# Optimization experiments

Hardware: AMD Instinct MI355X
Metric: run time of the kernel (lower is better)

Reference implementation:

```python
import jax, jax.numpy as jnp
import numpy as np
import math

INPUT_DIM = 1024
QUERY_DIM = 1024
VALUE_DIM = 1024

def setup_inputs() -> dict:
    key = jax.random.key(0)
    ks = jax.random.split(key, 7)
    N, T, D = 4, 4096, INPUT_DIM
    s_in = 1.0 / math.sqrt(D)
    X = jax.random.normal(ks[0], (N, T, D), dtype=jnp.float32)
    # torch.nn.Linear weights: (out, in), init ~ U(-1/sqrt(in), 1/sqrt(in))
    Wq = jax.random.uniform(ks[1], (QUERY_DIM, D), jnp.float32, -s_in, s_in)
    bq = jax.random.uniform(ks[2], (QUERY_DIM,), jnp.float32, -s_in, s_in)
    Wk = jax.random.uniform(ks[3], (QUERY_DIM, D), jnp.float32, -s_in, s_in)
    bk = jax.random.uniform(ks[4], (QUERY_DIM,), jnp.float32, -s_in, s_in)
    Wv = jax.random.uniform(ks[5], (VALUE_DIM, D), jnp.float32, -s_in, s_in)
    bv = jax.random.uniform(ks[6], (VALUE_DIM,), jnp.float32, -s_in, s_in)
    return {"X": X, "Wq": Wq, "bq": bq, "Wk": Wk, "bk": bk, "Wv": Wv, "bv": bv}

def reference(X, Wq, bq, Wk, bk, Wv, bv):
    N, T, D = X.shape
    q = jnp.einsum('ntd,qd->ntq', X, Wq) + bq  # (N,T,Q)
    k = jnp.einsum('ntd,qd->ntq', X, Wk) + bk  # (N,T,Q)
    v = jnp.einsum('ntd,vd->ntv', X, Wv) + bv  # (N,T,V)
    # NOTE: original scales by sqrt(D) = sqrt(input_dim), not sqrt(query_dim)
    scores = jnp.einsum('ntq,nsq->nts', q, k) / jnp.sqrt(jnp.asarray(D, X.dtype))
    attn = jax.nn.softmax(scores, axis=-1)  # (N,T,T)
    return jnp.einsum('nts,nsv->ntv', attn, v)
```

## Files before the change

kernel.cpp:

```cpp
#include <hip/hip_runtime.h>
#include <stdint.h>

typedef unsigned short u16;
typedef unsigned char u8;
typedef unsigned int u32;
typedef short shortx8 __attribute__((ext_vector_type(8)));
typedef float floatx4 __attribute__((ext_vector_type(4)));
typedef int intx4 __attribute__((ext_vector_type(4)));
typedef int intx8 __attribute__((ext_vector_type(8)));

__device__ __forceinline__ u16 f2bf(float f) {
    u32 u = __builtin_bit_cast(u32, f);
    u = (u + 0x7fffu + ((u >> 16) & 1u)) >> 16;
    return (u16)u;
}

#if defined(__has_builtin)
#  if __has_builtin(__builtin_amdgcn_cvt_pk_fp8_f32)
#    define HAVE_CVT_FP8 1
#  endif
#  if __has_builtin(__builtin_amdgcn_global_load_lds)
#    define HAVE_GLL 1
#  endif
#endif
#ifndef HAVE_CVT_FP8
#  define HAVE_CVT_FP8 0
#endif
#ifndef HAVE_GLL
#  define HAVE_GLL 0
#endif

__device__ __forceinline__ u8 f2fp8(float f) {
#if HAVE_CVT_FP8
    return (u8)(__builtin_amdgcn_cvt_pk_fp8_f32(f, f, 0, false) & 0xff);
#else
    u32 u = __builtin_bit_cast(u32, f);
    u32 s = (u >> 24) & 0x80u;
    u32 m = u & 0x7fffffffu;
    if (m >= 0x43e00000u) return (u8)(s | 0x7eu);
    if (m < 0x3c800000u) {
        int q = __float2int_rn(__builtin_bit_cast(float, m) * 512.f);
        return (u8)(s | (u32)q);
    }
    u32 r = m + 0x7ffffu + ((m >> 20) & 1u);
    u32 code = (((r >> 23) - 120u) << 3) | ((r >> 20) & 7u);
    if (code > 0x7eu) code = 0x7eu;
    return (u8)(s | code);
#endif
}

#if HAVE_GLL
__device__ __forceinline__ void gload_lds16(const void* g, void* l) {
    __builtin_amdgcn_global_load_lds(
        (const __attribute__((address_space(1))) u32*)g,
        (__attribute__((address_space(3))) u32*)l,
        16, 0, 0);
}
#endif

template <typename OutT, int MODE, int SWZ>
__global__ __launch_bounds__(256, 2) void gemm_bt(
    const u16* __restrict__ Ag, const u16* __restrict__ Bg, OutT* __restrict__ Cg,
    int lda, int ldb, int ldc, int K,
    const float* __restrict__ aux, float scale,
    long long sAz, long long sBz, long long sCz, long long sXz,
    int swz_nhalf)
{
    __shared__ u16 smem[4][128 * 32];

    int z, mb, nb;
    if constexpr (SWZ) {
        const int f = blockIdx.x, xcd = f & 7, g = f >> 3;
        z = xcd >> 1;
        mb = g & 31;
        nb = (xcd & 1) * swz_nhalf + (g >> 5);
    } else {
        z = blockIdx.z; mb = blockIdx.y; nb = blockIdx.x;
    }
    const int m0 = mb * 128, n0 = nb * 128;

    const u16* A = Ag + (long long)z * sAz;
    const u16* B = Bg + (long long)z * sBz;
    OutT* C = Cg + (long long)z * sCz;
    const float* auxp = aux ? aux + (long long)z * sXz : nullptr;

    const int tid = threadIdx.x, lane = tid & 63, wv = tid >> 6;

    const int srow = lane >> 2;
    const int schunk = (lane & 3) * 8;
    const u16* gA0 = A + (size_t)(m0 + wv * 16 + srow) * lda + schunk;
    const u16* gA1 = gA0 + (size_t)64 * lda;
    const u16* gB0 = B + (size_t)(n0 + wv * 16 + srow) * ldb + schunk;
    const u16* gB1 = gB0 + (size_t)64 * ldb;
    const int wb = wv * 512;

    const int wm = (wv & 1) * 64, wn = (wv >> 1) * 64;
    const int mi = lane & 15, kq = lane >> 4;

    floatx4 acc[4][4] = {};

    for (int k0 = 0; k0 < K; k0 += 64) {
#if HAVE_GLL
        gload_lds16(gA0,      &smem[0][wb]);
        gload_lds16(gA1,      &smem[0][2048 + wb]);
        gload_lds16(gA0 + 32, &smem[1][wb]);
        gload_lds16(gA1 + 32, &smem[1][2048 + wb]);
        gload_lds16(gB0,      &smem[2][wb]);
        gload_lds16(gB1,      &smem[2][2048 + wb]);
        gload_lds16(gB0 + 32, &smem[3][wb]);
        gload_lds16(gB1 + 32, &smem[3][2048 + wb]);
#else
        *(shortx8*)(&smem[0][wb] + lane * 8)        = *(const shortx8*)gA0;
        *(shortx8*)(&smem[0][2048 + wb] + lane * 8) = *(const shortx8*)gA1;
        *(shortx8*)(&smem[1][wb] + lane * 8)        = *(const shortx8*)(gA0 + 32);
        *(shortx8*)(&smem[1][2048 + wb] + lane * 8) = *(const shortx8*)(gA1 + 32);
        *(shortx8*)(&smem[2][wb] + lane * 8)        = *(const shortx8*)gB0;
        *(shortx8*)(&smem[2][2048 + wb] + lane * 8) = *(const shortx8*)gB1;
        *(shortx8*)(&smem[3][wb] + lane * 8)        = *(const shortx8*)(gB0 + 32);
        *(shortx8*)(&smem[3][2048 + wb] + lane * 8) = *(const shortx8*)(gB1 + 32);
#endif
        gA0 += 64; gA1 += 64; gB0 += 64; gB1 += 64;
        __syncthreads();

#pragma unroll
        for (int h = 0; h < 2; h++) {
            const u16* Ap = smem[h];
            const u16* Bp = smem[2 + h];
            shortx8 af[4], bfr[4];
#pragma unroll
            for (int i = 0; i < 4; i++)
                af[i] = *(const shortx8*)(Ap + (wm + i * 16 + mi) * 32 + kq * 8);
#pragma unroll
            for (int j = 0; j < 4; j++)
                bfr[j] = *(const shortx8*)(Bp + (wn + j * 16 + mi) * 32 + kq * 8);
#pragma unroll
            for (int i = 0; i < 4; i++)
#pragma unroll
                for (int j = 0; j < 4; j++)
                    acc[i][j] = __builtin_amdgcn_mfma_f32_16x16x32_bf16(
                        af[i], bfr[j], acc[i][j], 0, 0, 0);
        }
        __syncthreads();
    }

    float cb[4];
    if constexpr (MODE == 1) {
#pragma unroll
        for (int j = 0; j < 4; j++) cb[j] = auxp[n0 + wn + j * 16 + mi];
    }

    if constexpr (sizeof(OutT) == 2) {
        u16* ct = &smem[0][0];
#pragma unroll
        for (int i = 0; i < 4; i++) {
#pragma unroll
            for (int r = 0; r < 4; r++) {
                const int lrow = wm + i * 16 + kq * 4 + r;
                float radd = 0.f;
                if constexpr (MODE == 2) radd = auxp[m0 + lrow];
#pragma unroll
                for (int j = 0; j < 4; j++) {
                    float v = acc[i][j][r];
                    if constexpr (MODE == 1) v += cb[j];
                    if constexpr (MODE == 2) v += radd;
                    ct[lrow * 128 + wn + j * 16 + mi] = f2bf(v);
                }
            }
        }
        __syncthreads();
#pragma unroll
        for (int it = 0; it < 8; it++) {
            const int fl = (it * 256 + tid) * 8;
            const int row = fl >> 7, col = fl & 127;
            *(uint4*)(C + (size_t)(m0 + row) * ldc + n0 + col) =
                *(const uint4*)(ct + fl);
        }
    } else if constexpr (sizeof(OutT) == 1) {
        u8* ct = (u8*)&smem[0][0];
#pragma unroll
        for (int i = 0; i < 4; i++) {
#pragma unroll
            for (int r = 0; r < 4; r++) {
                const int lrow = wm + i * 16 + kq * 4 + r;
#pragma unroll
                for (int j = 0; j < 4; j++) {
                    float v = acc[i][j][r];
                    if constexpr (MODE == 1) v += cb[j];
                    ct[lrow * 128 + wn + j * 16 + mi] = f2fp8(v);
                }
            }
        }
        __syncthreads();
        u8* base = (u8*)Cg + ((size_t)mb * 16 + nb) * 16384;
#pragma unroll
        for (int it = 0; it < 4; it++) {
            const int fl = (it * 256 + tid) * 16;
            const int row = fl >> 7, c = (fl >> 4) & 7;
            *(uint4*)(base + row * 128 + ((c ^ (row & 7)) << 4)) =
                *(const uint4*)(ct + fl);
        }
    } else {
#pragma unroll
        for (int i = 0; i < 4; i++) {
#pragma unroll
            for (int r = 0; r < 4; r++) {
                const int row = m0 + wm + i * 16 + kq * 4 + r;
                float rmul = 1.f;
                if constexpr (MODE == 4) rmul = 1.0f / auxp[row];
                OutT* crow = C + (size_t)row * ldc;
#pragma unroll
                for (int j = 0; j < 4; j++) {
                    const int col = n0 + wn + j * 16 + mi;
                    crow[col] = acc[i][j][r] * rmul;
                }
            }
        }
    }
}

__device__ __forceinline__ intx8 cat8(intx4 a, intx4 b) {
    return __builtin_shufflevector(a, b, 0, 1, 2, 3, 4, 5, 6, 7);
}

template <int SWZ>
__global__ __launch_bounds__(256, 1) void gemm_fp8_scores(
    const u8* __restrict__ QKt, u16* __restrict__ Pg,
    float* __restrict__ sums, float scale, int T)
{
    __shared__ u8 smem[2][16384];

    int z, mb, nb;
    if constexpr (SWZ) {
        const int f = blockIdx.x, xcd = f & 7, g = f >> 3;
        z = xcd >> 1;
        mb = g & 31;
        nb = (xcd & 1) * 16 + (g >> 5);
    } else {
        z = blockIdx.z; mb = blockIdx.y; nb = blockIdx.x;
    }
    const int m0 = mb * 128, n0 = nb * 128;

    const u8* At = QKt + ((size_t)(z * 32 + mb) * 16) * 16384;
    const u8* Bt = QKt + ((size_t)(z * 32 + nb) * 16 + 8) * 16384;
    u16* P = Pg + (size_t)z * T * T;
    float* sumz = sums + (size_t)z * T;

    const int tid = threadIdx.x, lane = tid & 63, wv = tid >> 6;
    const int wm = (wv & 1) * 64, wn = (wv >> 1) * 64;
    const int mi = lane & 15, kq = lane >> 4;
    const int xm = mi & 7;
    const int off0 = ((2 * kq) ^ xm) * 16;
    const int off1 = ((2 * kq + 1) ^ xm) * 16;

    const u8* gA = At + wv * 4096 + lane * 16;
    const u8* gB = Bt + wv * 4096 + lane * 16;
    u8* lA = &smem[0][wv * 4096];
    u8* lB = &smem[1][wv * 4096];

    floatx4 acc[4][4] = {};

    for (int kp = 0; kp < 8; kp++) {
#if HAVE_GLL
#pragma unroll
        for (int i = 0; i < 4; i++) {
            gload_lds16(gA + i * 1024, lA + i * 1024);
            gload_lds16(gB + i * 1024, lB + i * 1024);
        }
#else
#pragma unroll
        for (int i = 0; i < 4; i++) {
            *(uint4*)(lA + i * 1024 + lane * 16) = *(const uint4*)(gA + i * 1024);
            *(uint4*)(lB + i * 1024 + lane * 16) = *(const uint4*)(gB + i * 1024);
        }
#endif
        gA += 16384; gB += 16384;
        __syncthreads();

        intx8 af[4];
#pragma unroll
        for (int i = 0; i < 4; i++) {
            const u8* p = &smem[0][(wm + i * 16 + mi) * 128];
            af[i] = cat8(*(const intx4*)(p + off0), *(const intx4*)(p + off1));
        }
#pragma unroll
        for (int j = 0; j < 4; j++) {
            const u8* p = &smem[1][(wn + j * 16 + mi) * 128];
            const intx8 bfr = cat8(*(const intx4*)(p + off0), *(const intx4*)(p + off1));
#pragma unroll
            for (int i = 0; i < 4; i++)
                acc[i][j] = __builtin_amdgcn_mfma_scale_f32_16x16x128_f8f6f4(
                    af[i], bfr, acc[i][j], 0, 0,
                    0, 0x7f7f7f7f, 0, 0x7f7f7f7f);
        }
        __syncthreads();
    }

    u16* ct = (u16*)&smem[0][0];
#pragma unroll
    for (int i = 0; i < 4; i++) {
#pragma unroll
        for (int r = 0; r < 4; r++) {
            const int lrow = wm + i * 16 + kq * 4 + r;
            float rs = 0.f;
#pragma unroll
            for (int j = 0; j < 4; j++) {
                float v = __expf(acc[i][j][r] * scale);
                rs += v;
                ct[lrow * 128 + wn + j * 16 + mi] = f2bf(v);
            }
            rs += __shfl_xor(rs, 1);
            rs += __shfl_xor(rs, 2);
            rs += __shfl_xor(rs, 4);
            rs += __shfl_xor(rs, 8);
            if (mi == 0) atomicAdd(&sumz[m0 + lrow], rs);
        }
    }
    __syncthreads();
#pragma unroll
    for (int it = 0; it < 8; it++) {
        const int fl = (it * 256 + tid) * 8;
        const int row = fl >> 7, col = fl & 127;
        *(uint4*)(P + (size_t)(m0 + row) * T + n0 + col) = *(const uint4*)(ct + fl);
    }
}

__global__ __launch_bounds__(256) void cvt_bf16(const float* __restrict__ s,
                                                u16* __restrict__ d, int n8)
{
    int i = blockIdx.x * 256 + threadIdx.x;
    if (i >= n8) return;
    const float4* sp = (const float4*)s;
    float4 a = sp[2 * i], b = sp[2 * i + 1];
    uint4 o;
    o.x = (u32)f2bf(a.x) | ((u32)f2bf(a.y) << 16);
    o.y = (u32)f2bf(a.z) | ((u32)f2bf(a.w) << 16);
    o.z = (u32)f2bf(b.x) | ((u32)f2bf(b.y) << 16);
    o.w = (u32)f2bf(b.z) | ((u32)f2bf(b.w) << 16);
    *(uint4*)(d + 8 * i) = o;
}

__global__ void concat2(const float* __restrict__ a, const float* __restrict__ b,
                        float* __restrict__ d, int n)
{
    int i = blockIdx.x * 256 + threadIdx.x;
    if (i < n) d[i] = a[i];
    else if (i < 2 * n) d[i] = b[i - n];
}

extern "C" void kernel_launch(void* const* d_in, const int* in_sizes, int n_in,
                              void* d_out, int out_size, void* d_ws, size_t ws_size,
                              hipStream_t stream)
{
    const float* X  = (const float*)d_in[0];
    const float* Wq = (const float*)d_in[1];
    const float* bq = (const float*)d_in[2];
    const float* Wk = (const float*)d_in[3];
    const float* bk = (const float*)d_in[4];
    const float* Wv = (const float*)d_in[5];
    const float* bv = (const float*)d_in[6];
    float* out = (float*)d_out;

    const int T = 4096, NT = 4 * T;
    const long long TL = T;

    char* ws = (char*)d_ws;
    size_t off = 0;
    auto alloc = [&](size_t bytes) {
        char* p = ws + off;
        off += (bytes + 255) & ~(size_t)255;
        return p;
    };
    u16*   Wqk  = (u16*)alloc((size_t)2048 * 1024 * 2);
    u16*   Wvb  = (u16*)alloc((size_t)1024 * 1024 * 2);
    float* bqk  = (float*)alloc(2048 * 4);
    u8*    QKt  = (u8*)alloc((size_t)128 * 16 * 16384);
    u16*   Vt   = (u16*)alloc((size_t)1024 * NT * 2);
    float* sums = (float*)alloc((size_t)NT * 4);
    size_t pbase = off;
    u16*   Xb   = (u16*)alloc((size_t)NT * 1024 * 2);
    u16*   P    = Xb;

    const size_t need_batched = pbase + (size_t)4 * T * T * 2;
    const bool batched = ws_size >= need_batched;

    cvt_bf16<<<dim3((NT * 1024 / 8 + 255) / 256), dim3(256), 0, stream>>>(X, Xb, NT * 1024 / 8);
    cvt_bf16<<<dim3(512), dim3(256), 0, stream>>>(Wq, Wqk, 1024 * 1024 / 8);
    cvt_bf16<<<dim3(512), dim3(256), 0, stream>>>(Wk, Wqk + 1024 * 1024, 1024 * 1024 / 8);
    cvt_bf16<<<dim3(512), dim3(256), 0, stream>>>(Wv, Wvb, 1024 * 1024 / 8);
    concat2<<<dim3(8), dim3(256), 0, stream>>>(bq, bk, bqk, 1024);
    hipMemsetAsync(sums, 0, (size_t)NT * 4, stream);

    gemm_bt<u8, 1, 0><<<dim3(16, 128, 1), dim3(256), 0, stream>>>(
        Xb, Wqk, QKt, 1024, 1024, 0, 1024, bqk, 0.f, 0, 0, 0, 0, 0);

    gemm_bt<u16, 2, 0><<<dim3(128, 8, 1), dim3(256), 0, stream>>>(
        Wvb, Xb, Vt, 1024, 1024, NT, 1024, bv, 0.f, 0, 0, 0, 0, 0);

    if (batched) {
        gemm_fp8_scores<1><<<dim3(4096), dim3(256), 0, stream>>>(
            QKt, P, sums, 0.03125f, T);
        gemm_bt<float, 4, 1><<<dim3(1024), dim3(256), 0, stream>>>(
            P, Vt, out, T, NT, 1024, T, sums, 0.f,
            TL * T, TL, TL * 1024, TL, 4);
    } else {
        for (int z = 0; z < 4; z++) {
            gemm_fp8_scores<0><<<dim3(32, 32, 1), dim3(256), 0, stream>>>(
                QKt + (size_t)z * 32 * 16 * 16384, P, sums + (size_t)z * T, 0.03125f, T);
            gemm_bt<float, 4, 0><<<dim3(8, 32, 1), dim3(256), 0, stream>>>(
                P, Vt + (size_t)z * T, out + (size_t)z * T * 1024,
                T, NT, 1024, T, sums + (size_t)z * T, 0.f, 0, 0, 0, 0, 0);
        }
    }
    (void)in_sizes; (void)n_in; (void)out_size;
}
```

Measured before the change: 578.0 us.

## Double-buffer LDS tiles in FP8 scores GEMM and regroup block swizzle

```diff
diff --git a/kernel.cpp b/kernel.cpp
--- a/kernel.cpp
+++ b/kernel.cpp
@@ -227,14 +227,15 @@
     const u8* __restrict__ QKt, u16* __restrict__ Pg,
     float* __restrict__ sums, float scale, int T)
 {
-    __shared__ u8 smem[2][16384];
+    __shared__ u8 smem[4][16384];
 
     int z, mb, nb;
     if constexpr (SWZ) {
         const int f = blockIdx.x, xcd = f & 7, g = f >> 3;
         z = xcd >> 1;
-        mb = g & 31;
-        nb = (xcd & 1) * 16 + (g >> 5);
+        const int s = g >> 7, t = g & 127;
+        mb = (s << 3) | (t & 7);
+        nb = (xcd & 1) * 16 + (t >> 3);
     } else {
         z = blockIdx.z; mb = blockIdx.y; nb = blockIdx.x;
     }
@@ -254,37 +255,57 @@
 
     const u8* gA = At + wv * 4096 + lane * 16;
     const u8* gB = Bt + wv * 4096 + lane * 16;
-    u8* lA = &smem[0][wv * 4096];
-    u8* lB = &smem[1][wv * 4096];
 
     floatx4 acc[4][4] = {};
 
+#if HAVE_GLL
+#pragma unroll
+    for (int i = 0; i < 4; i++) {
+        gload_lds16(gA + i * 1024, &smem[0][wv * 4096] + i * 1024);
+        gload_lds16(gB + i * 1024, &smem[1][wv * 4096] + i * 1024);
+    }
+#else
+#pragma unroll
+    for (int i = 0; i < 4; i++) {
+        *(uint4*)(&smem[0][wv * 4096] + i * 1024 + lane * 16) = *(const uint4*)(gA + i * 1024);
+        *(uint4*)(&smem[1][wv * 4096] + i * 1024 + lane * 16) = *(const uint4*)(gB + i * 1024);
+    }
+#endif
+    gA += 16384; gB += 16384;
+    __syncthreads();
+
+    int cur = 0;
     for (int kp = 0; kp < 8; kp++) {
+        const int nxt = cur ^ 2;
+        if (kp < 7) {
 #if HAVE_GLL
 #pragma unroll
+            for (int i = 0; i < 4; i++) {
+                gload_lds16(gA + i * 1024, &smem[nxt][wv * 4096] + i * 1024);
+                gload_lds16(gB + i * 1024, &smem[nxt + 1][wv * 4096] + i * 1024);
+            }
+#else
+#pragma unroll
+            for (int i = 0; i < 4; i++) {
+                *(uint4*)(&smem[nxt][wv * 4096] + i * 1024 + lane * 16) = *(const uint4*)(gA + i * 1024);
+                *(uint4*)(&smem[nxt + 1][wv * 4096] + i * 1024 + lane * 16) = *(const uint4*)(gB + i * 1024);
+            }
+#endif
+            gA += 16384; gB += 16384;
+        }
+        __builtin_amdgcn_sched_barrier(0);
+
+        const u8* Ap = &smem[cur][0];
+        const u8* Bp = &smem[cur + 1][0];
+        intx8 af[4];
+#pragma unroll
         for (int i = 0; i < 4; i++) {
-            gload_lds16(gA + i * 1024, lA + i * 1024);
-            gload_lds16(gB + i * 1024, lB + i * 1024);
-        }
-#else
-#pragma unroll
-        for (int i = 0; i < 4; i++) {
-            *(uint4*)(lA + i * 1024 + lane * 16) = *(const uint4*)(gA + i * 1024);
-            *(uint4*)(lB + i * 1024 + lane * 16) = *(const uint4*)(gB + i * 1024);
-        }
-#endif
-        gA += 16384; gB += 16384;
-        __syncthreads();
-
-        intx8 af[4];
-#pragma unroll
-        for (int i = 0; i < 4; i++) {
-            const u8* p = &smem[0][(wm + i * 16 + mi) * 128];
+            const u8* p = Ap + (wm + i * 16 + mi) * 128;
             af[i] = cat8(*(const intx4*)(p + off0), *(const intx4*)(p + off1));
         }
 #pragma unroll
         for (int j = 0; j < 4; j++) {
-            const u8* p = &smem[1][(wn + j * 16 + mi) * 128];
+            const u8* p = Bp + (wn + j * 16 + mi) * 128;
             const intx8 bfr = cat8(*(const intx4*)(p + off0), *(const intx4*)(p + off1));
 #pragma unroll
             for (int i = 0; i < 4; i++)
@@ -293,6 +314,7 @@
                     0, 0x7f7f7f7f, 0, 0x7f7f7f7f);
         }
         __syncthreads();
+        cur = nxt;
     }
 
     u16* ct = (u16*)&smem[0][0];
```

Result: faster. 535.1 us (-7.4%).
